# Performance work log

Measured on AMD Instinct MI355X. Metric: run time of the kernel, lower is better.

Reference implementation:

```python
import jax, jax.numpy as jnp
import numpy as np

L, N, C = 128, 32, 128
DIM_MLP, OUT = 128, 128


def setup_inputs() -> dict:
    key = jax.random.key(0)
    ks = jax.random.split(key, 6)
    s_in2 = 1.0 / np.sqrt(2 * C)
    s_mid = 1.0 / np.sqrt(DIM_MLP)
    s_in = 1.0 / np.sqrt(C)
    return {
        "x": jax.random.normal(ks[0], (L, N, C), jnp.float32),
        "attn_w1": jax.random.normal(ks[1], (2 * C, DIM_MLP), jnp.float32) * s_in2,
        "attn_b1": jnp.zeros((DIM_MLP,), jnp.float32),
        "attn_w2": jax.random.normal(ks[2], (DIM_MLP, OUT), jnp.float32) * s_mid,
        "attn_b2": jnp.zeros((OUT,), jnp.float32),
        "value_w1": jax.random.normal(ks[3], (C, DIM_MLP), jnp.float32) * s_in,
        "value_b1": jnp.zeros((DIM_MLP,), jnp.float32),
        "value_w2": jax.random.normal(ks[4], (DIM_MLP, OUT), jnp.float32) * s_mid,
        "value_b2": jnp.zeros((OUT,), jnp.float32),
    }


def reference(x, attn_w1, attn_b1, attn_w2, attn_b2,
              value_w1, value_b1, value_w2, value_b2):
    l, n, c = x.shape
    # Outer concat: pair[i, j, b] = concat(x[i, b], x[j, b])  -> (l, l, N, 2C)
    xi = jnp.broadcast_to(x[:, None, :, :], (l, l, n, c))
    xj = jnp.broadcast_to(x[None, :, :, :], (l, l, n, c))
    pair = jnp.concatenate([xi, xj], axis=-1)
    # Pairwise attention MLP (ReLU hidden, linear output)
    h = jax.nn.relu(pair @ attn_w1 + attn_b1)          # (l, l, N, dim_mlp)
    attn = h @ attn_w2 + attn_b2                       # (l, l, N, out)
    # Value MLP
    hv = jax.nn.relu(x @ value_w1 + value_b1)          # (l, N, dim_mlp)
    value = hv @ value_w2 + value_b2                   # (l, N, out)
    # Elementwise weighted reduce over key axis j (NOT a matmul over channels)
    out = jnp.einsum('ijbc,jbc->ibc', attn, value)     # (l, N, out)
    return out
```

## Files before the change

### kernel.cpp

```cpp
#include <hip/hip_runtime.h>
#include <hip/hip_bf16.h>

#define L_DIM 128
#define N_DIM 32
#define C_DIM 128
#define K_DIM 128
#define OUT_DIM 128

#define QV_STRIDE 132

typedef __attribute__((ext_vector_type(8))) short short8;
typedef __attribute__((ext_vector_type(4))) float float4v;

static __device__ __forceinline__ short bf16_bits(float f) {
    __bf16 h = (__bf16)f;
    return __builtin_bit_cast(short, h);
}

__global__ __launch_bounds__(256) void k_pre(
    const float* __restrict__ x,
    const float* __restrict__ attn_w1, const float* __restrict__ attn_b1,
    const float* __restrict__ attn_w2,
    const float* __restrict__ value_w1, const float* __restrict__ value_b1,
    const float* __restrict__ value_w2, const float* __restrict__ value_b2,
    float* __restrict__ P, float* __restrict__ Q, float* __restrict__ V,
    short* __restrict__ W2s)
{
    int bid = blockIdx.x;
    if (bid >= 512) {
        int e = (bid - 512) * 256 + threadIdx.x;
        int idx  = e & 7;
        int colr = (e >> 3) & 15;
        int quad = (e >> 7) & 3;
        int mi   = (e >> 9) & 3;
        int ct   = e >> 11;
        int k = quad * 8 + 32 * mi + idx;
        int c = ct * 16 + colr;
        W2s[e] = bf16_bits(attn_w2[k * OUT_DIM + c]);
        return;
    }

    __shared__ float xs[8][C_DIM];
    __shared__ float hvs[8][K_DIM];
    int tid = threadIdx.x;
    int r0  = bid * 8;

    {
        int f = tid * 4;
        int row = f >> 7, c = f & 127;
        *(float4v*)(&xs[row][c]) = *(const float4v*)(x + (r0 + row) * C_DIM + c);
    }
    __syncthreads();

    int ks   = tid & 127;
    int half = tid >> 7;

    float pacc[4] = {0,0,0,0};
    float qacc[4] = {0,0,0,0};
    float hacc[4] = {0,0,0,0};
    #pragma unroll 4
    for (int c = 0; c < C_DIM; ++c) {
        float wa = attn_w1[c * K_DIM + ks];
        float wb = attn_w1[(C_DIM + c) * K_DIM + ks];
        float wv = value_w1[c * K_DIM + ks];
        #pragma unroll
        for (int r = 0; r < 4; ++r) {
            float xr = xs[half * 4 + r][c];
            pacc[r] = fmaf(xr, wa, pacc[r]);
            qacc[r] = fmaf(xr, wb, qacc[r]);
            hacc[r] = fmaf(xr, wv, hacc[r]);
        }
    }
    float b1 = attn_b1[ks], vb1 = value_b1[ks];
    #pragma unroll
    for (int r = 0; r < 4; ++r) {
        int rr = r0 + half * 4 + r;
        int i = rr >> 5, bb = rr & 31;
        P[(bb * L_DIM + i) * K_DIM + ks] = pacc[r];
        Q[(bb * L_DIM + i) * K_DIM + ks] = qacc[r] + b1;
        hvs[half * 4 + r][ks] = fmaxf(hacc[r] + vb1, 0.f);
    }
    __syncthreads();

    float vacc[4] = {0,0,0,0};
    #pragma unroll 4
    for (int k = 0; k < K_DIM; ++k) {
        float w = value_w2[k * OUT_DIM + ks];
        #pragma unroll
        for (int r = 0; r < 4; ++r)
            vacc[r] = fmaf(hvs[half * 4 + r][k], w, vacc[r]);
    }
    float vb2 = value_b2[ks];
    #pragma unroll
    for (int r = 0; r < 4; ++r) {
        int rr = r0 + half * 4 + r;
        int i = rr >> 5, bb = rr & 31;
        V[(bb * L_DIM + i) * OUT_DIM + ks] = vacc[r] + vb2;
    }
}

__global__ __launch_bounds__(512, 4)
void k_main(
    const float* __restrict__ P, const float* __restrict__ Q,
    const float* __restrict__ V,
    const short* __restrict__ W2s, const float* __restrict__ attn_b2,
    float* __restrict__ out)
{
    __shared__ short A_lds[2 * 256 * 8];
    __shared__ float Q_lds[2][16 * QV_STRIDE];
    __shared__ float V_lds[2][16 * QV_STRIDE];
    __shared__ float P_lds[2 * K_DIM];

    int b     = blockIdx.x >> 6;
    int ipair = blockIdx.x & 63;
    int tid   = threadIdx.x;
    int wave  = tid >> 6;
    int lane  = tid & 63;
    int quad  = lane >> 4;
    int col   = lane & 15;
    int iw    = wave >> 2;
    int ctq   = wave & 3;

    short8 bfrag[2][4];
    const short8* w2p = (const short8*)W2s;
    #pragma unroll
    for (int cl = 0; cl < 2; ++cl)
        #pragma unroll
        for (int mi = 0; mi < 4; ++mi)
            bfrag[cl][mi] = w2p[(((ctq * 2 + cl) * 4 + mi) * 4 + quad) * 16 + col];

    if (tid < 64)
        *(float4v*)&P_lds[tid * 4] =
            *(const float4v*)(P + (b * L_DIM + ipair * 2 + (tid >> 5)) * K_DIM
                              + (tid & 31) * 4);

    int srow = tid >> 5;
    int sc   = (tid & 31) * 4;
    const float* Qbase = Q + (size_t)(b * L_DIM) * K_DIM;
    const float* Vbase = V + (size_t)(b * L_DIM) * OUT_DIM;

    {
        float4v q4 = *(const float4v*)(Qbase + srow * K_DIM + sc);
        float4v v4 = *(const float4v*)(Vbase + srow * OUT_DIM + sc);
        *(float4v*)&Q_lds[0][srow * QV_STRIDE + sc] = q4;
        *(float4v*)&V_lds[0][srow * QV_STRIDE + sc] = v4;
    }
    __syncthreads();

    int bi = tid >> 8;
    int bj = (tid >> 4) & 15;
    int bk = tid & 15;

    float acc0 = 0.f, acc1 = 0.f, sv0 = 0.f, sv1 = 0.f;
    int cc0 = ctq * 32 + col;
    int cc1 = cc0 + 16;

    for (int r = 0; r < 8; ++r) {
        int cur = r & 1;

        {
            const float* Qc = &Q_lds[cur][bj * QV_STRIDE + bk * 8];
            float4v q0 = *(const float4v*)Qc;
            float4v q1 = *(const float4v*)(Qc + 4);
            const float* Pc = &P_lds[bi * K_DIM + bk * 8];
            float4v p0 = *(const float4v*)Pc;
            float4v p1 = *(const float4v*)(Pc + 4);
            float4v s0 = p0 + q0;
            float4v s1 = p1 + q1;
            short8 a;
            #pragma unroll
            for (int t = 0; t < 4; ++t) {
                a[t]     = bf16_bits(fmaxf(s0[t], 0.f));
                a[t + 4] = bf16_bits(fmaxf(s1[t], 0.f));
            }
            *(short8*)&A_lds[(bi * 256 + bk * 16 + (bj ^ bk)) * 8] = a;
        }

        float4v nq, nv;
        if (r < 7) {
            nq = *(const float4v*)(Qbase + ((r + 1) * 16 + srow) * K_DIM + sc);
            nv = *(const float4v*)(Vbase + ((r + 1) * 16 + srow) * OUT_DIM + sc);
        }

        __syncthreads();

        int nxt = cur ^ 1;
        if (r < 7) {
            *(float4v*)&Q_lds[nxt][srow * QV_STRIDE + sc] = nq;
            *(float4v*)&V_lds[nxt][srow * QV_STRIDE + sc] = nv;
        }

        float4v c40 = {0.f, 0.f, 0.f, 0.f};
        float4v c41 = {0.f, 0.f, 0.f, 0.f};
        #pragma unroll
        for (int ks = 0; ks < 4; ++ks) {
            int kq = ks * 4 + quad;
            short8 af = *(const short8*)
                &A_lds[(iw * 256 + kq * 16 + (col ^ kq)) * 8];
            c40 = __builtin_amdgcn_mfma_f32_16x16x32_bf16(
                    af, bfrag[0][ks], c40, 0, 0, 0);
            c41 = __builtin_amdgcn_mfma_f32_16x16x32_bf16(
                    af, bfrag[1][ks], c41, 0, 0, 0);
        }
        const float* Vc = &V_lds[cur][0];
        #pragma unroll
        for (int rr = 0; rr < 4; ++rr) {
            float v0 = Vc[(quad * 4 + rr) * QV_STRIDE + cc0];
            float v1 = Vc[(quad * 4 + rr) * QV_STRIDE + cc1];
            acc0 = fmaf(c40[rr], v0, acc0);  sv0 += v0;
            acc1 = fmaf(c41[rr], v1, acc1);  sv1 += v1;
        }

        __syncthreads();
    }

    acc0 += __shfl_xor(acc0, 16, 64);  acc0 += __shfl_xor(acc0, 32, 64);
    acc1 += __shfl_xor(acc1, 16, 64);  acc1 += __shfl_xor(acc1, 32, 64);
    sv0  += __shfl_xor(sv0, 16, 64);   sv0  += __shfl_xor(sv0, 32, 64);
    sv1  += __shfl_xor(sv1, 16, 64);   sv1  += __shfl_xor(sv1, 32, 64);

    if (quad == 0) {
        int ig = ipair * 2 + iw;
        out[(ig * N_DIM + b) * OUT_DIM + cc0] = acc0 + attn_b2[cc0] * sv0;
        out[(ig * N_DIM + b) * OUT_DIM + cc1] = acc1 + attn_b2[cc1] * sv1;
    }
}

extern "C" void kernel_launch(void* const* d_in, const int* in_sizes, int n_in,
                              void* d_out, int out_size, void* d_ws, size_t ws_size,
                              hipStream_t stream)
{
    const float* x        = (const float*)d_in[0];
    const float* attn_w1  = (const float*)d_in[1];
    const float* attn_b1  = (const float*)d_in[2];
    const float* attn_w2  = (const float*)d_in[3];
    const float* attn_b2  = (const float*)d_in[4];
    const float* value_w1 = (const float*)d_in[5];
    const float* value_b1 = (const float*)d_in[6];
    const float* value_w2 = (const float*)d_in[7];
    const float* value_b2 = (const float*)d_in[8];
    float* out = (float*)d_out;

    float* ws  = (float*)d_ws;
    float* P   = ws;
    float* Q   = ws + 524288;
    float* V   = ws + 1048576;
    short* W2s = (short*)(ws + 1572864);

    k_pre<<<576, 256, 0, stream>>>(x, attn_w1, attn_b1, attn_w2,
                                   value_w1, value_b1, value_w2, value_b2,
                                   P, Q, V, W2s);
    k_main<<<2048, 512, 0, stream>>>(P, Q, V, W2s, attn_b2, out);
}
```

Measured before the change: 132.3 us.

## Build MFMA A fragments in registers and halve block size in k_main

```diff
diff --git a/kernel.cpp b/kernel.cpp
--- a/kernel.cpp
+++ b/kernel.cpp
@@ -99,14 +99,14 @@
     }
 }
 
-__global__ __launch_bounds__(512, 4)
+__global__ __launch_bounds__(256)
+__attribute__((amdgpu_waves_per_eu(3)))
 void k_main(
     const float* __restrict__ P, const float* __restrict__ Q,
     const float* __restrict__ V,
     const short* __restrict__ W2s, const float* __restrict__ attn_b2,
     float* __restrict__ out)
 {
-    __shared__ short A_lds[2 * 256 * 8];
     __shared__ float Q_lds[2][16 * QV_STRIDE];
     __shared__ float V_lds[2][16 * QV_STRIDE];
     __shared__ float P_lds[2 * K_DIM];
@@ -118,53 +118,63 @@
     int lane  = tid & 63;
     int quad  = lane >> 4;
     int col   = lane & 15;
-    int iw    = wave >> 2;
-    int ctq   = wave & 3;
-
-    short8 bfrag[2][4];
+    int iw    = wave >> 1;
+    int cth   = wave & 1;
+
+    short8 bfrag[4][4];
     const short8* w2p = (const short8*)W2s;
     #pragma unroll
-    for (int cl = 0; cl < 2; ++cl)
+    for (int cl = 0; cl < 4; ++cl)
         #pragma unroll
         for (int mi = 0; mi < 4; ++mi)
-            bfrag[cl][mi] = w2p[(((ctq * 2 + cl) * 4 + mi) * 4 + quad) * 16 + col];
+            bfrag[cl][mi] =
+                w2p[(((cth * 4 + cl) * 4 + mi) * 4 + quad) * 16 + col];
 
     if (tid < 64)
         *(float4v*)&P_lds[tid * 4] =
             *(const float4v*)(P + (b * L_DIM + ipair * 2 + (tid >> 5)) * K_DIM
                               + (tid & 31) * 4);
 
-    int srow = tid >> 5;
-    int sc   = (tid & 31) * 4;
+    int srow = tid >> 4;
+    int sc8  = (tid & 15) * 8;
     const float* Qbase = Q + (size_t)(b * L_DIM) * K_DIM;
     const float* Vbase = V + (size_t)(b * L_DIM) * OUT_DIM;
 
     {
-        float4v q4 = *(const float4v*)(Qbase + srow * K_DIM + sc);
-        float4v v4 = *(const float4v*)(Vbase + srow * OUT_DIM + sc);
-        *(float4v*)&Q_lds[0][srow * QV_STRIDE + sc] = q4;
-        *(float4v*)&V_lds[0][srow * QV_STRIDE + sc] = v4;
+        const float* qp = Qbase + srow * K_DIM + sc8;
+        const float* vp = Vbase + srow * OUT_DIM + sc8;
+        float4v qa = *(const float4v*)qp, qb = *(const float4v*)(qp + 4);
+        float4v va = *(const float4v*)vp, vb = *(const float4v*)(vp + 4);
+        *(float4v*)&Q_lds[0][srow * QV_STRIDE + sc8]     = qa;
+        *(float4v*)&Q_lds[0][srow * QV_STRIDE + sc8 + 4] = qb;
+        *(float4v*)&V_lds[0][srow * QV_STRIDE + sc8]     = va;
+        *(float4v*)&V_lds[0][srow * QV_STRIDE + sc8 + 4] = vb;
     }
     __syncthreads();
 
-    int bi = tid >> 8;
-    int bj = (tid >> 4) & 15;
-    int bk = tid & 15;
-
-    float acc0 = 0.f, acc1 = 0.f, sv0 = 0.f, sv1 = 0.f;
-    int cc0 = ctq * 32 + col;
-    int cc1 = cc0 + 16;
+    float acc[4] = {0.f, 0.f, 0.f, 0.f};
+    float sv[4]  = {0.f, 0.f, 0.f, 0.f};
+    const float* Pw = &P_lds[iw * K_DIM];
 
     for (int r = 0; r < 8; ++r) {
         int cur = r & 1;
 
-        {
-            const float* Qc = &Q_lds[cur][bj * QV_STRIDE + bk * 8];
-            float4v q0 = *(const float4v*)Qc;
-            float4v q1 = *(const float4v*)(Qc + 4);
-            const float* Pc = &P_lds[bi * K_DIM + bk * 8];
-            float4v p0 = *(const float4v*)Pc;
-            float4v p1 = *(const float4v*)(Pc + 4);
+        float4v nqa, nqb, nva, nvb;
+        if (r < 7) {
+            const float* qp = Qbase + ((r + 1) * 16 + srow) * K_DIM + sc8;
+            const float* vp = Vbase + ((r + 1) * 16 + srow) * OUT_DIM + sc8;
+            nqa = *(const float4v*)qp; nqb = *(const float4v*)(qp + 4);
+            nva = *(const float4v*)vp; nvb = *(const float4v*)(vp + 4);
+        }
+
+        short8 af[4];
+        const float* Qc = &Q_lds[cur][col * QV_STRIDE + quad * 8];
+        #pragma unroll
+        for (int ksl = 0; ksl < 4; ++ksl) {
+            float4v q0 = *(const float4v*)(Qc + ksl * 32);
+            float4v q1 = *(const float4v*)(Qc + ksl * 32 + 4);
+            float4v p0 = *(const float4v*)(Pw + ksl * 32 + quad * 8);
+            float4v p1 = *(const float4v*)(Pw + ksl * 32 + quad * 8 + 4);
             float4v s0 = p0 + q0;
             float4v s1 = p1 + q1;
             short8 a;
@@ -173,56 +183,51 @@
                 a[t]     = bf16_bits(fmaxf(s0[t], 0.f));
                 a[t + 4] = bf16_bits(fmaxf(s1[t], 0.f));
             }
-            *(short8*)&A_lds[(bi * 256 + bk * 16 + (bj ^ bk)) * 8] = a;
-        }
-
-        float4v nq, nv;
+            af[ksl] = a;
+        }
+
+        const float* Vc = &V_lds[cur][0];
+        #pragma unroll
+        for (int cl = 0; cl < 4; ++cl) {
+            float4v c4 = {0.f, 0.f, 0.f, 0.f};
+            #pragma unroll
+            for (int ksl = 0; ksl < 4; ++ksl)
+                c4 = __builtin_amdgcn_mfma_f32_16x16x32_bf16(
+                        af[ksl], bfrag[cl][ksl], c4, 0, 0, 0);
+            int cc = cth * 64 + cl * 16 + col;
+            #pragma unroll
+            for (int rr = 0; rr < 4; ++rr) {
+                float v = Vc[(quad * 4 + rr) * QV_STRIDE + cc];
+                acc[cl] = fmaf(c4[rr], v, acc[cl]);
+                sv[cl] += v;
+            }
+        }
+
         if (r < 7) {
-            nq = *(const float4v*)(Qbase + ((r + 1) * 16 + srow) * K_DIM + sc);
-            nv = *(const float4v*)(Vbase + ((r + 1) * 16 + srow) * OUT_DIM + sc);
-        }
-
-        __syncthreads();
-
-        int nxt = cur ^ 1;
-        if (r < 7) {
-            *(float4v*)&Q_lds[nxt][srow * QV_STRIDE + sc] = nq;
-            *(float4v*)&V_lds[nxt][srow * QV_STRIDE + sc] = nv;
-        }
-
-        float4v c40 = {0.f, 0.f, 0.f, 0.f};
-        float4v c41 = {0.f, 0.f, 0.f, 0.f};
-        #pragma unroll
-        for (int ks = 0; ks < 4; ++ks) {
-            int kq = ks * 4 + quad;
-            short8 af = *(const short8*)
-                &A_lds[(iw * 256 + kq * 16 + (col ^ kq)) * 8];
-            c40 = __builtin_amdgcn_mfma_f32_16x16x32_bf16(
-                    af, bfrag[0][ks], c40, 0, 0, 0);
-            c41 = __builtin_amdgcn_mfma_f32_16x16x32_bf16(
-                    af, bfrag[1][ks], c41, 0, 0, 0);
-        }
-        const float* Vc = &V_lds[cur][0];
-        #pragma unroll
-        for (int rr = 0; rr < 4; ++rr) {
-            float v0 = Vc[(quad * 4 + rr) * QV_STRIDE + cc0];
-            float v1 = Vc[(quad * 4 + rr) * QV_STRIDE + cc1];
-            acc0 = fmaf(c40[rr], v0, acc0);  sv0 += v0;
-            acc1 = fmaf(c41[rr], v1, acc1);  sv1 += v1;
-        }
-
-        __syncthreads();
-    }
-
-    acc0 += __shfl_xor(acc0, 16, 64);  acc0 += __shfl_xor(acc0, 32, 64);
-    acc1 += __shfl_xor(acc1, 16, 64);  acc1 += __shfl_xor(acc1, 32, 64);
-    sv0  += __shfl_xor(sv0, 16, 64);   sv0  += __shfl_xor(sv0, 32, 64);
-    sv1  += __shfl_xor(sv1, 16, 64);   sv1  += __shfl_xor(sv1, 32, 64);
+            int nxt = cur ^ 1;
+            *(float4v*)&Q_lds[nxt][srow * QV_STRIDE + sc8]     = nqa;
+            *(float4v*)&Q_lds[nxt][srow * QV_STRIDE + sc8 + 4] = nqb;
+            *(float4v*)&V_lds[nxt][srow * QV_STRIDE + sc8]     = nva;
+            *(float4v*)&V_lds[nxt][srow * QV_STRIDE + sc8 + 4] = nvb;
+            __syncthreads();
+        }
+    }
+
+    #pragma unroll
+    for (int cl = 0; cl < 4; ++cl) {
+        acc[cl] += __shfl_xor(acc[cl], 16, 64);
+        acc[cl] += __shfl_xor(acc[cl], 32, 64);
+        sv[cl]  += __shfl_xor(sv[cl], 16, 64);
+        sv[cl]  += __shfl_xor(sv[cl], 32, 64);
+    }
 
     if (quad == 0) {
         int ig = ipair * 2 + iw;
-        out[(ig * N_DIM + b) * OUT_DIM + cc0] = acc0 + attn_b2[cc0] * sv0;
-        out[(ig * N_DIM + b) * OUT_DIM + cc1] = acc1 + attn_b2[cc1] * sv1;
+        #pragma unroll
+        for (int cl = 0; cl < 4; ++cl) {
+            int cc = cth * 64 + cl * 16 + col;
+            out[(ig * N_DIM + b) * OUT_DIM + cc] = acc[cl] + attn_b2[cc] * sv[cl];
+        }
     }
 }
 
@@ -250,5 +255,5 @@
     k_pre<<<576, 256, 0, stream>>>(x, attn_w1, attn_b1, attn_w2,
                                    value_w1, value_b1, value_w2, value_b2,
                                    P, Q, V, W2s);
-    k_main<<<2048, 512, 0, stream>>>(P, Q, V, W2s, attn_b2, out);
-}
+    k_main<<<2048, 256, 0, stream>>>(P, Q, V, W2s, attn_b2, out);
+}
```

Measured after the change: 127.4 us. 3.7% less time.
